# Optimization experiments

Measured on AMD Instinct MI355X. Metric: run time of the kernel, lower is better.

The kernel has to match this reference:

```python
import jax, jax.numpy as jnp
import numpy as np
import math

B, N, DIM = 8, 4096, 768
H, D = 12, 64
STAGES = 3
LN_EPS = 1e-5

def _ln(x, g, b):
    mu = jnp.mean(x, axis=-1, keepdims=True)
    var = jnp.mean(jnp.square(x - mu), axis=-1, keepdims=True)
    return (x - mu) * jax.lax.rsqrt(var + LN_EPS) * g + b

def _mlp(x, W, b, g, be):
    return jax.nn.gelu(_ln(x @ W + b, g, be), approximate=False)

def setup_inputs() -> dict:
    key = jax.random.key(0)
    ks = jax.random.split(key, 16)
    s = lambda i, shape, sc: jax.random.normal(ks[i], shape, jnp.float32) * sc
    return {
        "x": s(0, (B, N, DIM), 1.0),
        "Wq": s(1, (DIM, H * D), DIM ** -0.5),
        "Wk": s(2, (DIM, H * D), DIM ** -0.5),
        "Wv": s(3, (DIM, H * D), DIM ** -0.5),
        "pool_W": s(4, (STAGES, D, D), D ** -0.5),
        "pool_b": jnp.zeros((STAGES, D), jnp.float32),
        "pool_g": jnp.ones((STAGES, D), jnp.float32),
        "pool_be": jnp.zeros((STAGES, D), jnp.float32),
        "exp_W": s(5, (STAGES, D, D), D ** -0.5),
        "exp_b": jnp.zeros((STAGES, D), jnp.float32),
        "exp_g": jnp.ones((STAGES, D), jnp.float32),
        "exp_be": jnp.zeros((STAGES, D), jnp.float32),
        "Wo": s(6, (H * D, DIM), (H * D) ** -0.5),
        "bo": jnp.zeros((DIM,), jnp.float32),
    }

def reference(x, Wq, Wk, Wv, pool_W, pool_b, pool_g, pool_be,
              exp_W, exp_b, exp_g, exp_be, Wo, bo):
    b, n, _ = x.shape
    # project and split heads -> (b, h, n, d)
    def heads(y):
        return y.reshape(b, n, H, D).transpose(0, 2, 1, 3)
    q = heads(x @ Wq)
    k = heads(x @ Wk)
    v = heads(x @ Wv)
    fmap = lambda t: jax.nn.elu(t) + 1.0
    q = fmap(q)
    k = fmap(k)

    kc, vc = k, v
    for i in range(STAGES):
        s = kc.shape[2]
        if s > 1:
            pad = (-s) % 2
            if pad:
                kc = jnp.pad(kc, ((0, 0), (0, 0), (0, pad), (0, 0)))
                vc = jnp.pad(vc, ((0, 0), (0, 0), (0, pad), (0, 0)))
            kc = kc.reshape(b, H, -1, 2, D).mean(axis=3)
            kc = _mlp(kc, pool_W[i], pool_b[i], pool_g[i], pool_be[i])
            vc = vc.reshape(b, H, -1, 2, D).mean(axis=3)

    kc = kc / math.sqrt(kc.shape[2])
    kv = jnp.einsum('bhnd,bhne->bhde', kc, vc)       # (b,h,d,d)
    out = jnp.einsum('bhnd,bhde->bhne', q, kv)       # (b,h,n,d)
    k_sum = kc.sum(axis=2, keepdims=True)            # (b,h,1,d)
    q_k_sum = jnp.sum(q * k_sum, axis=-1, keepdims=True)  # (b,h,n,1)
    out = out / (q_k_sum + 1e-6)

    for i in reversed(range(STAGES)):
        out = _mlp(out, exp_W[i], exp_b[i], exp_g[i], exp_be[i])

    out = out.transpose(0, 2, 1, 3).reshape(b, n, H * D)
    return out @ Wo + bo
```

## Files before the change

kernel.cpp:

```cpp
#include <hip/hip_runtime.h>
#include <math.h>

#define B_   8
#define N_   4096
#define DIM_ 768
#define H_   12
#define D_   64

typedef unsigned short ushort_t;
typedef unsigned int uint_t;
typedef __attribute__((ext_vector_type(8))) short short8;
typedef __attribute__((ext_vector_type(4))) float f32x4;

__device__ __forceinline__ float gelu_exact(float z) {
  return 0.5f * z * (1.f + erff(z * 0.70710678118654752440f));
}

__device__ __forceinline__ ushort_t f2bf(float f) {
  union { float f; unsigned u; } x; x.f = f;
  unsigned r = x.u + 0x7FFFu + ((x.u >> 16) & 1u);
  return (ushort_t)(r >> 16);
}

__device__ __forceinline__ float bf2f(ushort_t h) {
  union { unsigned u; float f; } x; x.u = ((unsigned)h) << 16;
  return x.f;
}

__device__ __forceinline__ void gl_lds16(const ushort_t* g, ushort_t* l) {
  __builtin_amdgcn_global_load_lds(
      (const __attribute__((address_space(1))) void*)g,
      (__attribute__((address_space(3))) void*)l, 16, 0, 0);
}

__global__ __launch_bounds__(256) void transpose_w_bf16(
    const float* __restrict__ src, ushort_t* __restrict__ dst)
{
  __shared__ float t[32][33];
  const int lx = threadIdx.x & 31, ly = threadIdx.x >> 5;
  const int bx = blockIdx.x * 32;
  const int by = blockIdx.y * 32;
  #pragma unroll
  for (int j = 0; j < 32; j += 8)
    t[ly + j][lx] = src[(size_t)(by + ly + j) * 768 + bx + lx];
  __syncthreads();
  #pragma unroll
  for (int j = 0; j < 32; j += 8)
    dst[(size_t)(bx + ly + j) * 768 + by + lx] = f2bf(t[lx][ly + j]);
}

__global__ __launch_bounds__(256) void transpose64_bf16(
    const float* __restrict__ pW, const float* __restrict__ eW,
    ushort_t* __restrict__ dst)
{
  const int m = blockIdx.x;
  const float* src = (m < 3) ? (pW + m * 4096) : (eW + (m - 3) * 4096);
  ushort_t* o = dst + m * 4096;
  for (int i = threadIdx.x; i < 4096; i += 256) {
    const int r = i >> 6, c = i & 63;
    o[c * 64 + r] = f2bf(src[r * 64 + c]);
  }
}

__global__ __launch_bounds__(256) void conv_f32_bf16(
    const float* __restrict__ src, ushort_t* __restrict__ dst)
{
  const int i = blockIdx.x * 256 + threadIdx.x;
  float4 f = ((const float4*)src)[i];
  ushort4 o;
  o.x = f2bf(f.x); o.y = f2bf(f.y); o.z = f2bf(f.z); o.w = f2bf(f.w);
  ((ushort4*)dst)[i] = o;
}

#define GEMM_MAINLOOP(A, Bt, K)                                               \
  __shared__ ushort_t As[128 * 32];                                           \
  __shared__ ushort_t Bs[128 * 32];                                           \
  const int tid = threadIdx.x;                                                \
  const int row0 = blockIdx.y * 128;                                          \
  const int col0 = blockIdx.x * 128;                                          \
  const int sr = tid >> 2;                                                    \
  const int sk = (tid & 3) * 8;                                               \
  const ushort_t* Ag0 = (A) + (size_t)(row0 + sr) * (K) + sk;                 \
  const ushort_t* Ag1 = Ag0 + (size_t)64 * (K);                               \
  const ushort_t* Bg0 = (Bt) + (size_t)(col0 + sr) * (K) + sk;                \
  const ushort_t* Bg1 = Bg0 + (size_t)64 * (K);                               \
  ushort_t* Asw = As + (tid >> 6) * 512;                                      \
  ushort_t* Bsw = Bs + (tid >> 6) * 512;                                      \
  const int w = tid >> 6, lane = tid & 63;                                    \
  const int wm = w >> 1, wn = w & 1;                                          \
  const int qd = lane >> 4, l15 = lane & 15;                                  \
  const int aoff = (wm * 64 + l15) * 32 + qd * 8;                             \
  const int boff = (wn * 64 + l15) * 32 + qd * 8;                             \
  f32x4 acc[4][4] = {};                                                       \
  for (int k0 = 0; k0 < (K); k0 += 32) {                                      \
    __syncthreads();                                                          \
    gl_lds16(Ag0 + k0, Asw);                                                  \
    gl_lds16(Ag1 + k0, Asw + 2048);                                           \
    gl_lds16(Bg0 + k0, Bsw);                                                  \
    gl_lds16(Bg1 + k0, Bsw + 2048);                                           \
    __syncthreads();                                                          \
    short8 af[4], bfr[4];                                                     \
    _Pragma("unroll")                                                         \
    for (int mt = 0; mt < 4; ++mt) af[mt] = *(const short8*)&As[aoff + mt * 512]; \
    _Pragma("unroll")                                                         \
    for (int nt = 0; nt < 4; ++nt) bfr[nt] = *(const short8*)&Bs[boff + nt * 512]; \
    _Pragma("unroll")                                                         \
    for (int mt = 0; mt < 4; ++mt)                                            \
      _Pragma("unroll")                                                       \
      for (int nt = 0; nt < 4; ++nt)                                          \
        acc[mt][nt] = __builtin_amdgcn_mfma_f32_16x16x32_bf16(                \
            af[mt], bfr[nt], acc[mt][nt], 0, 0, 0);                           \
  }

__global__ __launch_bounds__(256) void gemm_qkv(
    const ushort_t* __restrict__ A, const ushort_t* __restrict__ Bt,
    ushort_t* __restrict__ qo, ushort_t* __restrict__ ko, float* __restrict__ vco)
{
  GEMM_MAINLOOP(A, Bt, 768)
  const int sel = col0 / 768;
  const int colbase = (col0 % 768) + wn * 64;
  if (sel < 2) {
    ushort_t* o = (sel == 0) ? qo : ko;
    #pragma unroll
    for (int mt = 0; mt < 4; ++mt) {
      #pragma unroll
      for (int nt = 0; nt < 4; ++nt) {
        const int cg = colbase + nt * 16 + l15;
        #pragma unroll
        for (int r = 0; r < 4; ++r) {
          const int rg = row0 + wm * 64 + mt * 16 + qd * 4 + r;
          const float vv = acc[mt][nt][r];
          const float e = (vv > 0.f) ? vv + 1.f : expf(vv);
          o[(size_t)rg * 768 + cg] = f2bf(e);
        }
      }
    }
  } else {
    const int b = row0 >> 12;
    const int hh = colbase >> 6;
    const int n8base = ((row0 & 4095) >> 3) + wm * 8 + (qd >> 1);
    #pragma unroll
    for (int mt = 0; mt < 4; ++mt) {
      #pragma unroll
      for (int nt = 0; nt < 4; ++nt) {
        float s = acc[mt][nt][0] + acc[mt][nt][1] + acc[mt][nt][2] + acc[mt][nt][3];
        s += __shfl_xor(s, 16, 64);
        if (!(qd & 1)) {
          const int n8 = n8base + mt * 2;
          const int d = nt * 16 + l15;
          vco[(((size_t)b * 12 + hh) * 512 + n8) * 64 + d] = 0.125f * s;
        }
      }
    }
  }
}

__global__ __launch_bounds__(256) void gemm_out(
    const ushort_t* __restrict__ A, const ushort_t* __restrict__ Bt,
    const float* __restrict__ bo, float* __restrict__ C)
{
  GEMM_MAINLOOP(A, Bt, 768)
  #pragma unroll
  for (int mt = 0; mt < 4; ++mt) {
    #pragma unroll
    for (int nt = 0; nt < 4; ++nt) {
      const int cg = col0 + wn * 64 + nt * 16 + l15;
      #pragma unroll
      for (int r = 0; r < 4; ++r) {
        const int rg = row0 + wm * 64 + mt * 16 + qd * 4 + r;
        C[(size_t)rg * 768 + cg] = acc[mt][nt][r] + bo[cg];
      }
    }
  }
}

__global__ __launch_bounds__(256) void pool_mfma(
    const ushort_t* __restrict__ in, ushort_t* __restrict__ out,
    int n_out, long h_stride, int ts, long in_bs, long out_bs,
    const ushort_t* __restrict__ Wt, const float* __restrict__ bias,
    const float* __restrict__ g, const float* __restrict__ be)
{
  __shared__ ushort_t Wl[64 * 72];
  __shared__ ushort_t tl[128 * 72];
  const int tid = threadIdx.x;
  const int h = blockIdx.y;
  const int bb = blockIdx.z;
  const int row0 = blockIdx.x * 128;
  in  += (size_t)bb * in_bs;
  out += (size_t)bb * out_bs;

  {
    const uint_t* ws = (const uint_t*)Wt;
    for (int i = tid; i < 2048; i += 256) {
      const int r = i >> 5, c = i & 31;
      ((uint_t*)(Wl + r * 72))[c] = ws[i];
    }
  }
  #pragma unroll
  for (int j = 0; j < 4; ++j) {
    const int idx = j * 256 + tid;
    const int rl = idx >> 3, ch = idx & 7;
    const ushort_t* p = in + (size_t)h * h_stride + (size_t)(2 * (row0 + rl)) * ts + ch * 8;
    short8 a = *(const short8*)p;
    short8 b2 = *(const short8*)(p + ts);
    short8 o;
    #pragma unroll
    for (int e = 0; e < 8; ++e)
      o[e] = (short)f2bf(0.5f * (bf2f((ushort_t)a[e]) + bf2f((ushort_t)b2[e])));
    *(short8*)&tl[rl * 72 + ch * 8] = o;
  }
  __syncthreads();

  const int w = tid >> 6, lane = tid & 63;
  const int quad = lane >> 4, l15 = lane & 15;

  float bv[4], gv[4], bev[4];
  #pragma unroll
  for (int nt = 0; nt < 4; ++nt) {
    const int c = nt * 16 + l15;
    bv[nt] = bias[c]; gv[nt] = g[c]; bev[nt] = be[c];
  }
  f32x4 a2[2][4];
  #pragma unroll
  for (int mt = 0; mt < 2; ++mt)
    #pragma unroll
    for (int nt = 0; nt < 4; ++nt)
      a2[mt][nt] = f32x4{bv[nt], bv[nt], bv[nt], bv[nt]};

  #pragma unroll
  for (int ks = 0; ks < 2; ++ks) {
    short8 af[2], bfr[4];
    #pragma unroll
    for (int mt = 0; mt < 2; ++mt)
      af[mt] = *(const short8*)&tl[(w * 32 + mt * 16 + l15) * 72 + ks * 32 + quad * 8];
    #pragma unroll
    for (int nt = 0; nt < 4; ++nt)
      bfr[nt] = *(const short8*)&Wl[(nt * 16 + l15) * 72 + ks * 32 + quad * 8];
    #pragma unroll
    for (int mt = 0; mt < 2; ++mt)
      #pragma unroll
      for (int nt = 0; nt < 4; ++nt)
        a2[mt][nt] = __builtin_amdgcn_mfma_f32_16x16x32_bf16(af[mt], bfr[nt], a2[mt][nt], 0, 0, 0);
  }

  #pragma unroll
  for (int mt = 0; mt < 2; ++mt)
    #pragma unroll
    for (int r = 0; r < 4; ++r) {
      float sum = a2[mt][0][r] + a2[mt][1][r] + a2[mt][2][r] + a2[mt][3][r];
      #pragma unroll
      for (int m = 1; m < 16; m <<= 1) sum += __shfl_xor(sum, m, 64);
      const float mu = sum * 0.015625f;
      float dv[4], var = 0.f;
      #pragma unroll
      for (int nt = 0; nt < 4; ++nt) { dv[nt] = a2[mt][nt][r] - mu; var += dv[nt] * dv[nt]; }
      #pragma unroll
      for (int m = 1; m < 16; m <<= 1) var += __shfl_xor(var, m, 64);
      const float rstd = rsqrtf(var * 0.015625f + 1e-5f);
      const int rg = row0 + w * 32 + mt * 16 + quad * 4 + r;
      #pragma unroll
      for (int nt = 0; nt < 4; ++nt) {
        const float z = dv[nt] * rstd * gv[nt] + bev[nt];
        out[((size_t)h * n_out + rg) * 64 + nt * 16 + l15] = f2bf(gelu_exact(z));
      }
    }
}

__global__ __launch_bounds__(256) void kv_part_kernel(
    const ushort_t* __restrict__ kc, const float* __restrict__ vc,
    float* __restrict__ kvp, float* __restrict__ ksp)
{
  __shared__ float ks[32 * 64];
  __shared__ float vs[32 * 64];
  const int tid = threadIdx.x;
  const int h = blockIdx.x;
  const int c = blockIdx.y;
  const int bb = blockIdx.z;
  kc  += (size_t)bb * 393216;
  vc  += (size_t)bb * 393216;
  kvp += (size_t)bb * 786432;
  ksp += (size_t)bb * 12288;
  const ushort_t* kp = kc + ((size_t)h * 512 + c * 32) * 64;
  const float* vp = vc + ((size_t)h * 512 + c * 32) * 64;
  #pragma unroll
  for (int i = 0; i < 2; ++i) {
    ushort4 u = ((const ushort4*)kp)[tid + 256 * i];
    float4 f; f.x = bf2f(u.x); f.y = bf2f(u.y); f.z = bf2f(u.z); f.w = bf2f(u.w);
    ((float4*)ks)[tid + 256 * i] = f;
    ((float4*)vs)[tid + 256 * i] = ((const float4*)vp)[tid + 256 * i];
  }
  __syncthreads();

  const int e = tid & 63;
  const int dg = tid >> 6;
  float acc[16] = {};
  float accs = 0.f;
  for (int nn = 0; nn < 32; ++nn) {
    const float vv = vs[nn * 64 + e];
    #pragma unroll
    for (int j = 0; j < 16; ++j)
      acc[j] += ks[nn * 64 + dg * 16 + j] * vv;
    if (tid < 64) accs += ks[nn * 64 + tid];
  }
  float* o = kvp + ((size_t)h * 16 + c) * 4096;
  #pragma unroll
  for (int j = 0; j < 16; ++j)
    o[(dg * 16 + j) * 64 + e] = acc[j];
  if (tid < 64) ksp[(h * 16 + c) * 64 + tid] = accs;
}

__global__ __launch_bounds__(256) void kv_reduce_t(
    const float* __restrict__ kvp, const float* __restrict__ ksp,
    ushort_t* __restrict__ kvxT)
{
  const int bb = blockIdx.y;
  kvp  += (size_t)bb * 786432;
  ksp  += (size_t)bb * 12288;
  kvxT += (size_t)bb * 61440;
  const int idx = blockIdx.x * 256 + threadIdx.x;
  const int h = idx / 5120;
  const int rem = idx - h * 5120;
  const int er = rem >> 6, d = rem & 63;
  const float scale = 0.044194173824159216f;
  float val = 0.f;
  if (er < 64) {
    float s = 0.f;
    #pragma unroll
    for (int c = 0; c < 16; ++c) s += kvp[((size_t)h * 16 + c) * 4096 + d * 64 + er];
    val = s * scale;
  } else if (er == 64) {
    float s = 0.f;
    #pragma unroll
    for (int c = 0; c < 16; ++c) s += ksp[(h * 16 + c) * 64 + d];
    val = s * scale;
  }
  kvxT[idx] = f2bf(val);
}

__global__ __launch_bounds__(256) void attn_exp_mfma(
    const ushort_t* __restrict__ q16, const ushort_t* __restrict__ kvxT,
    const ushort_t* __restrict__ eWt,
    const float* __restrict__ eb, const float* __restrict__ eg,
    const float* __restrict__ ebe, ushort_t* __restrict__ out16)
{
  __shared__ ushort_t kvl[80 * 72];
  __shared__ ushort_t Wl[3 * 64 * 72];
  __shared__ ushort_t tl[128 * 72];
  const int tid = threadIdx.x;
  const int h = blockIdx.y;
  const int bb = blockIdx.z;
  const int row0 = blockIdx.x * 128;
  q16   += (size_t)bb * 3145728;
  out16 += (size_t)bb * 3145728;
  kvxT  += (size_t)bb * 61440;

  {
    const uint_t* src = (const uint_t*)(kvxT + (size_t)h * 5120);
    for (int i = tid; i < 2560; i += 256) {
      const int r = i >> 5, c = i & 31;
      ((uint_t*)(kvl + r * 72))[c] = src[i];
    }
    const uint_t* ws = (const uint_t*)eWt;
    for (int i = tid; i < 6144; i += 256) {
      const int s = i >> 11, rem = i & 2047, r = rem >> 5, c = rem & 31;
      ((uint_t*)(Wl + (s * 64 + r) * 72))[c] = ws[i];
    }
  }
  __syncthreads();

  const int w = tid >> 6, lane = tid & 63;
  const int quad = lane >> 4, l15 = lane & 15;

  f32x4 acc[2][5] = {};
  #pragma unroll
  for (int ks = 0; ks < 2; ++ks) {
    short8 af[2], bfr[5];
    #pragma unroll
    for (int mt = 0; mt < 2; ++mt) {
      const int rg = row0 + w * 32 + mt * 16 + l15;
      af[mt] = *(const short8*)(q16 + (size_t)rg * 768 + h * 64 + ks * 32 + quad * 8);
    }
    #pragma unroll
    for (int nt = 0; nt < 5; ++nt)
      bfr[nt] = *(const short8*)&kvl[(nt * 16 + l15) * 72 + ks * 32 + quad * 8];
    #pragma unroll
    for (int mt = 0; mt < 2; ++mt)
      #pragma unroll
      for (int nt = 0; nt < 5; ++nt)
        acc[mt][nt] = __builtin_amdgcn_mfma_f32_16x16x32_bf16(af[mt], bfr[nt], acc[mt][nt], 0, 0, 0);
  }

  float t[2][4][4];
  #pragma unroll
  for (int mt = 0; mt < 2; ++mt)
    #pragma unroll
    for (int r = 0; r < 4; ++r) {
      const float den = __shfl(acc[mt][4][r], lane & 48, 64) + 1e-6f;
      const float inv = 1.f / den;
      #pragma unroll
      for (int nt = 0; nt < 4; ++nt)
        t[mt][nt][r] = acc[mt][nt][r] * inv;
    }

  for (int s = 2; s >= 0; --s) {
    __syncthreads();
    #pragma unroll
    for (int mt = 0; mt < 2; ++mt)
      #pragma unroll
      for (int nt = 0; nt < 4; ++nt)
        #pragma unroll
        for (int r = 0; r < 4; ++r)
          tl[(w * 32 + mt * 16 + quad * 4 + r) * 72 + nt * 16 + l15] = f2bf(t[mt][nt][r]);
    __syncthreads();

    float bv[4], gv[4], bev[4];
    #pragma unroll
    for (int nt = 0; nt < 4; ++nt) {
      const int c = s * 64 + nt * 16 + l15;
      bv[nt] = eb[c]; gv[nt] = eg[c]; bev[nt] = ebe[c];
    }
    f32x4 a2[2][4];
    #pragma unroll
    for (int mt = 0; mt < 2; ++mt)
      #pragma unroll
      for (int nt = 0; nt < 4; ++nt)
        a2[mt][nt] = f32x4{bv[nt], bv[nt], bv[nt], bv[nt]};

    #pragma unroll
    for (int ks = 0; ks < 2; ++ks) {
      short8 af[2], bfr[4];
      #pragma unroll
      for (int mt = 0; mt < 2; ++mt)
        af[mt] = *(const short8*)&tl[(w * 32 + mt * 16 + l15) * 72 + ks * 32 + quad * 8];
      #pragma unroll
      for (int nt = 0; nt < 4; ++nt)
        bfr[nt] = *(const short8*)&Wl[(s * 64 + nt * 16 + l15) * 72 + ks * 32 + quad * 8];
      #pragma unroll
      for (int mt = 0; mt < 2; ++mt)
        #pragma unroll
        for (int nt = 0; nt < 4; ++nt)
          a2[mt][nt] = __builtin_amdgcn_mfma_f32_16x16x32_bf16(af[mt], bfr[nt], a2[mt][nt], 0, 0, 0);
    }

    #pragma unroll
    for (int mt = 0; mt < 2; ++mt)
      #pragma unroll
      for (int r = 0; r < 4; ++r) {
        float sum = a2[mt][0][r] + a2[mt][1][r] + a2[mt][2][r] + a2[mt][3][r];
        #pragma unroll
        for (int m = 1; m < 16; m <<= 1) sum += __shfl_xor(sum, m, 64);
        const float mu = sum * 0.015625f;
        float dv[4], var = 0.f;
        #pragma unroll
        for (int nt = 0; nt < 4; ++nt) { dv[nt] = a2[mt][nt][r] - mu; var += dv[nt] * dv[nt]; }
        #pragma unroll
        for (int m = 1; m < 16; m <<= 1) var += __shfl_xor(var, m, 64);
        const float rstd = rsqrtf(var * 0.015625f + 1e-5f);
        #pragma unroll
        for (int nt = 0; nt < 4; ++nt) {
          const float z = dv[nt] * rstd * gv[nt] + bev[nt];
          t[mt][nt][r] = gelu_exact(z);
        }
      }
  }

  #pragma unroll
  for (int mt = 0; mt < 2; ++mt)
    #pragma unroll
    for (int nt = 0; nt < 4; ++nt)
      #pragma unroll
      for (int r = 0; r < 4; ++r) {
        const int rg = row0 + w * 32 + mt * 16 + quad * 4 + r;
        out16[(size_t)rg * 768 + h * 64 + nt * 16 + l15] = f2bf(t[mt][nt][r]);
      }
}

extern "C" void kernel_launch(void* const* d_in, const int* in_sizes, int n_in,
                              void* d_out, int out_size, void* d_ws, size_t ws_size,
                              hipStream_t stream)
{
  const float* x   = (const float*)d_in[0];
  const float* Wq  = (const float*)d_in[1];
  const float* Wk  = (const float*)d_in[2];
  const float* Wv  = (const float*)d_in[3];
  const float* pW  = (const float*)d_in[4];
  const float* pb  = (const float*)d_in[5];
  const float* pg  = (const float*)d_in[6];
  const float* pbe = (const float*)d_in[7];
  const float* eW  = (const float*)d_in[8];
  const float* eb  = (const float*)d_in[9];
  const float* eg  = (const float*)d_in[10];
  const float* ebe = (const float*)d_in[11];
  const float* Wo  = (const float*)d_in[12];
  const float* bo  = (const float*)d_in[13];
  float* outp = (float*)d_out;

  unsigned char* wsb = (unsigned char*)d_ws;
  ushort_t* WqkvT = (ushort_t*)(wsb + 0);
  ushort_t* WoT   = (ushort_t*)(wsb + 3538944);
  ushort_t* Wt6   = (ushort_t*)(wsb + 4718592);
  const size_t CB   = 4767744;
  const size_t PERB = 26075136;

  int NB;
  if      (ws_size >= CB + 8 * PERB) NB = 8;
  else if (ws_size >= CB + 4 * PERB) NB = 4;
  else if (ws_size >= CB + 2 * PERB) NB = 2;
  else if (ws_size >= CB + 1 * PERB) NB = 1;
  else return;

  unsigned char* cb = wsb + CB;
  ushort_t* xb16 = (ushort_t*)(cb);
  ushort_t* q16  = (ushort_t*)(cb + (size_t)NB *  6291456);
  ushort_t* k16  = (ushort_t*)(cb + (size_t)NB * 12582912);
  float*    vc   = (float*)   (cb + (size_t)NB * 18874368);
  ushort_t* kc_a = (ushort_t*)(cb + (size_t)NB * 20447232);
  ushort_t* kc_b = (ushort_t*)(cb + (size_t)NB * 23592960);
  ushort_t* kc_c = (ushort_t*)(cb + (size_t)NB * 25165824);
  ushort_t* kvxT = (ushort_t*)(cb + (size_t)NB * 25952256);
  float* kvp = (float*)k16;
  float* ksp = (float*)((unsigned char*)k16 + (size_t)NB * 3145728);
  ushort_t* ao16 = xb16;

  const ushort_t* pWt = Wt6;
  const ushort_t* eWt = Wt6 + 3 * 4096;
  const size_t SB = (size_t)N_ * DIM_;

  transpose_w_bf16<<<dim3(24, 24), 256, 0, stream>>>(Wq, WqkvT);
  transpose_w_bf16<<<dim3(24, 24), 256, 0, stream>>>(Wk, WqkvT + 768 * 768);
  transpose_w_bf16<<<dim3(24, 24), 256, 0, stream>>>(Wv, WqkvT + 2 * 768 * 768);
  transpose_w_bf16<<<dim3(24, 24), 256, 0, stream>>>(Wo, WoT);
  transpose64_bf16<<<6, 256, 0, stream>>>(pW, eW, Wt6);

  for (int b0 = 0; b0 < B_; b0 += NB) {
    const float* xc = x + (size_t)b0 * SB;
    float* oc = outp + (size_t)b0 * SB;

    conv_f32_bf16<<<NB * 3072, 256, 0, stream>>>(xc, xb16);
    gemm_qkv<<<dim3(18, NB * 32), 256, 0, stream>>>(xb16, WqkvT, q16, k16, vc);

    pool_mfma<<<dim3(16, 12, NB), 256, 0, stream>>>(k16, kc_a, 2048, 64L, 768,
        3145728L, 1572864L, pWt, pb, pg, pbe);
    pool_mfma<<<dim3(8, 12, NB), 256, 0, stream>>>(kc_a, kc_b, 1024, 131072L, 64,
        1572864L, 786432L, pWt + 4096, pb + 64, pg + 64, pbe + 64);
    pool_mfma<<<dim3(4, 12, NB), 256, 0, stream>>>(kc_b, kc_c, 512, 65536L, 64,
        786432L, 393216L, pWt + 8192, pb + 128, pg + 128, pbe + 128);

    kv_part_kernel<<<dim3(12, 16, NB), 256, 0, stream>>>(kc_c, vc, kvp, ksp);
    kv_reduce_t<<<dim3(240, NB), 256, 0, stream>>>(kvp, ksp, kvxT);

    attn_exp_mfma<<<dim3(32, 12, NB), 256, 0, stream>>>(q16, kvxT, eWt,
                                                        eb, eg, ebe, ao16);

    gemm_out<<<dim3(6, NB * 32), 256, 0, stream>>>(ao16, WoT, bo, oc);
  }
}
```

Baseline: 705.4 us.

## Double-buffer GEMM LDS tiles and remap workgroup IDs across XCDs

The shared GEMM main loop now uses two LDS buffers per operand. The global-to-LDS load for the next 32-wide K slice is issued before the MFMA compute on the current slice, so load latency can overlap compute. The workgroup index is also permuted in groups of 8 so that neighbouring tiles land on the same XCD, aiming for better L2 reuse. This doubles LDS use per block, which may lower occupancy, and the remap assumes the grid size is divisible by 8.

```diff
diff --git a/kernel.cpp b/kernel.cpp
--- a/kernel.cpp
+++ b/kernel.cpp
@@ -72,44 +72,57 @@
   ((ushort4*)dst)[i] = o;
 }
 
+#define GEMM_STAGE(kk, As_, Bs_)                                              \
+    gl_lds16(Ag0 + (kk), (As_) + stoff_);                                     \
+    gl_lds16(Ag1 + (kk), (As_) + stoff_ + 2048);                              \
+    gl_lds16(Bg0 + (kk), (Bs_) + stoff_);                                     \
+    gl_lds16(Bg1 + (kk), (Bs_) + stoff_ + 2048);
+
+#define GEMM_COMPUTE(As_, Bs_)                                                \
+  { short8 af[4], bfr[4];                                                     \
+    _Pragma("unroll")                                                         \
+    for (int mt = 0; mt < 4; ++mt) af[mt] = *(const short8*)&(As_)[aoff + mt * 512]; \
+    _Pragma("unroll")                                                         \
+    for (int nt = 0; nt < 4; ++nt) bfr[nt] = *(const short8*)&(Bs_)[boff + nt * 512]; \
+    _Pragma("unroll")                                                         \
+    for (int mt = 0; mt < 4; ++mt)                                            \
+      _Pragma("unroll")                                                       \
+      for (int nt = 0; nt < 4; ++nt)                                          \
+        acc[mt][nt] = __builtin_amdgcn_mfma_f32_16x16x32_bf16(                \
+            af[mt], bfr[nt], acc[mt][nt], 0, 0, 0); }
+
 #define GEMM_MAINLOOP(A, Bt, K)                                               \
-  __shared__ ushort_t As[128 * 32];                                           \
-  __shared__ ushort_t Bs[128 * 32];                                           \
+  __shared__ ushort_t As0[128 * 32];                                          \
+  __shared__ ushort_t As1[128 * 32];                                          \
+  __shared__ ushort_t Bs0[128 * 32];                                          \
+  __shared__ ushort_t Bs1[128 * 32];                                          \
   const int tid = threadIdx.x;                                                \
-  const int row0 = blockIdx.y * 128;                                          \
-  const int col0 = blockIdx.x * 128;                                          \
+  const int nwg_ = (int)(gridDim.x * gridDim.y);                              \
+  const int wgid0_ = (int)(blockIdx.y * gridDim.x + blockIdx.x);              \
+  const int wgid_ = (wgid0_ & 7) * (nwg_ >> 3) + (wgid0_ >> 3);               \
+  const int row0 = (wgid_ / (int)gridDim.x) * 128;                            \
+  const int col0 = (wgid_ % (int)gridDim.x) * 128;                            \
   const int sr = tid >> 2;                                                    \
   const int sk = (tid & 3) * 8;                                               \
   const ushort_t* Ag0 = (A) + (size_t)(row0 + sr) * (K) + sk;                 \
   const ushort_t* Ag1 = Ag0 + (size_t)64 * (K);                               \
   const ushort_t* Bg0 = (Bt) + (size_t)(col0 + sr) * (K) + sk;                \
   const ushort_t* Bg1 = Bg0 + (size_t)64 * (K);                               \
-  ushort_t* Asw = As + (tid >> 6) * 512;                                      \
-  ushort_t* Bsw = Bs + (tid >> 6) * 512;                                      \
+  const int stoff_ = (tid >> 6) * 512;                                        \
   const int w = tid >> 6, lane = tid & 63;                                    \
   const int wm = w >> 1, wn = w & 1;                                          \
   const int qd = lane >> 4, l15 = lane & 15;                                  \
   const int aoff = (wm * 64 + l15) * 32 + qd * 8;                             \
   const int boff = (wn * 64 + l15) * 32 + qd * 8;                             \
   f32x4 acc[4][4] = {};                                                       \
-  for (int k0 = 0; k0 < (K); k0 += 32) {                                      \
+  GEMM_STAGE(0, As0, Bs0)                                                     \
+  for (int k0 = 0; k0 < (K); k0 += 64) {                                      \
     __syncthreads();                                                          \
-    gl_lds16(Ag0 + k0, Asw);                                                  \
-    gl_lds16(Ag1 + k0, Asw + 2048);                                           \
-    gl_lds16(Bg0 + k0, Bsw);                                                  \
-    gl_lds16(Bg1 + k0, Bsw + 2048);                                           \
+    GEMM_STAGE(k0 + 32, As1, Bs1)                                             \
+    GEMM_COMPUTE(As0, Bs0)                                                    \
     __syncthreads();                                                          \
-    short8 af[4], bfr[4];                                                     \
-    _Pragma("unroll")                                                         \
-    for (int mt = 0; mt < 4; ++mt) af[mt] = *(const short8*)&As[aoff + mt * 512]; \
-    _Pragma("unroll")                                                         \
-    for (int nt = 0; nt < 4; ++nt) bfr[nt] = *(const short8*)&Bs[boff + nt * 512]; \
-    _Pragma("unroll")                                                         \
-    for (int mt = 0; mt < 4; ++mt)                                            \
-      _Pragma("unroll")                                                       \
-      for (int nt = 0; nt < 4; ++nt)                                          \
-        acc[mt][nt] = __builtin_amdgcn_mfma_f32_16x16x32_bf16(                \
-            af[mt], bfr[nt], acc[mt][nt], 0, 0, 0);                           \
+    if (k0 + 64 < (K)) { GEMM_STAGE(k0 + 64, As0, Bs0) }                      \
+    GEMM_COMPUTE(As1, Bs1)                                                    \
   }
 
 __global__ __launch_bounds__(256) void gemm_qkv(
```

New measurement: 698.0 us. Within noise of the previous version (-1.0%).

## Pool x before V projection and remap GEMM workgroups across XCDs

Applied to the files above, without the earlier changes.

Since V is only used after three stages of mean-pooling by 2, x is now averaged over groups of 8 rows first. The V projection then runs on an 8x smaller input in a separate small GEMM, which removes 1/3 of the QKV GEMM's FLOPs. The GEMM macro also remaps workgroup IDs so consecutive tiles interleave across the 8 XCDs, and the ELU path uses the fast __expf. Averaging bf16 x before the bf16 conversion changes rounding slightly, and the new kernel adds an extra pass over x.

```diff
diff --git a/kernel.cpp b/kernel.cpp
--- a/kernel.cpp
+++ b/kernel.cpp
@@ -72,12 +72,34 @@
   ((ushort4*)dst)[i] = o;
 }
 
+__global__ __launch_bounds__(256) void pool8_x(
+    const ushort_t* __restrict__ xb, ushort_t* __restrict__ x8)
+{
+  const int idx = blockIdx.x * 256 + threadIdx.x;
+  const int r = idx / 96, gc = idx - r * 96;
+  const ushort_t* p = xb + (size_t)(8 * r) * 768 + gc * 8;
+  float s[8] = {};
+  #pragma unroll
+  for (int j = 0; j < 8; ++j) {
+    short8 v = *(const short8*)(p + (size_t)j * 768);
+    #pragma unroll
+    for (int e = 0; e < 8; ++e) s[e] += bf2f((ushort_t)v[e]);
+  }
+  short8 o;
+  #pragma unroll
+  for (int e = 0; e < 8; ++e) o[e] = (short)f2bf(0.125f * s[e]);
+  *(short8*)(x8 + (size_t)r * 768 + gc * 8) = o;
+}
+
 #define GEMM_MAINLOOP(A, Bt, K)                                               \
   __shared__ ushort_t As[128 * 32];                                           \
   __shared__ ushort_t Bs[128 * 32];                                           \
   const int tid = threadIdx.x;                                                \
-  const int row0 = blockIdx.y * 128;                                          \
-  const int col0 = blockIdx.x * 128;                                          \
+  const int nwg_ = (int)(gridDim.x * gridDim.y);                              \
+  const int wgid0_ = (int)(blockIdx.y * gridDim.x + blockIdx.x);              \
+  const int wgid_ = (wgid0_ & 7) * (nwg_ >> 3) + (wgid0_ >> 3);               \
+  const int row0 = (wgid_ / (int)gridDim.x) * 128;                            \
+  const int col0 = (wgid_ % (int)gridDim.x) * 128;                            \
   const int sr = tid >> 2;                                                    \
   const int sk = (tid & 3) * 8;                                               \
   const ushort_t* Ag0 = (A) + (size_t)(row0 + sr) * (K) + sk;                 \
@@ -114,42 +136,44 @@
 
 __global__ __launch_bounds__(256) void gemm_qkv(
     const ushort_t* __restrict__ A, const ushort_t* __restrict__ Bt,
-    ushort_t* __restrict__ qo, ushort_t* __restrict__ ko, float* __restrict__ vco)
+    ushort_t* __restrict__ qo, ushort_t* __restrict__ ko)
 {
   GEMM_MAINLOOP(A, Bt, 768)
   const int sel = col0 / 768;
   const int colbase = (col0 % 768) + wn * 64;
-  if (sel < 2) {
-    ushort_t* o = (sel == 0) ? qo : ko;
-    #pragma unroll
-    for (int mt = 0; mt < 4; ++mt) {
-      #pragma unroll
-      for (int nt = 0; nt < 4; ++nt) {
-        const int cg = colbase + nt * 16 + l15;
-        #pragma unroll
-        for (int r = 0; r < 4; ++r) {
-          const int rg = row0 + wm * 64 + mt * 16 + qd * 4 + r;
-          const float vv = acc[mt][nt][r];
-          const float e = (vv > 0.f) ? vv + 1.f : expf(vv);
-          o[(size_t)rg * 768 + cg] = f2bf(e);
-        }
+  ushort_t* o = (sel == 0) ? qo : ko;
+  #pragma unroll
+  for (int mt = 0; mt < 4; ++mt) {
+    #pragma unroll
+    for (int nt = 0; nt < 4; ++nt) {
+      const int cg = colbase + nt * 16 + l15;
+      #pragma unroll
+      for (int r = 0; r < 4; ++r) {
+        const int rg = row0 + wm * 64 + mt * 16 + qd * 4 + r;
+        const float vv = acc[mt][nt][r];
+        const float e = (vv > 0.f) ? vv + 1.f : __expf(vv);
+        o[(size_t)rg * 768 + cg] = f2bf(e);
       }
     }
-  } else {
-    const int b = row0 >> 12;
-    const int hh = colbase >> 6;
-    const int n8base = ((row0 & 4095) >> 3) + wm * 8 + (qd >> 1);
-    #pragma unroll
-    for (int mt = 0; mt < 4; ++mt) {
-      #pragma unroll
-      for (int nt = 0; nt < 4; ++nt) {
-        float s = acc[mt][nt][0] + acc[mt][nt][1] + acc[mt][nt][2] + acc[mt][nt][3];
-        s += __shfl_xor(s, 16, 64);
-        if (!(qd & 1)) {
-          const int n8 = n8base + mt * 2;
-          const int d = nt * 16 + l15;
-          vco[(((size_t)b * 12 + hh) * 512 + n8) * 64 + d] = 0.125f * s;
-        }
+  }
+}
+
+__global__ __launch_bounds__(256) void gemm_v(
+    const ushort_t* __restrict__ A, const ushort_t* __restrict__ Bt,
+    float* __restrict__ vco)
+{
+  GEMM_MAINLOOP(A, Bt, 768)
+  #pragma unroll
+  for (int mt = 0; mt < 4; ++mt) {
+    #pragma unroll
+    for (int nt = 0; nt < 4; ++nt) {
+      const int cg = col0 + wn * 64 + nt * 16 + l15;
+      const int hh = cg >> 6, d = cg & 63;
+      #pragma unroll
+      for (int r = 0; r < 4; ++r) {
+        const int rg = row0 + wm * 64 + mt * 16 + qd * 4 + r;
+        const int b = rg >> 9, n = rg & 511;
+        vco[(((size_t)b * 12 + hh) * 512 + n) * 64 + d] = acc[mt][nt][r];
       }
     }
   }
@@ -500,7 +524,7 @@
   ushort_t* WoT   = (ushort_t*)(wsb + 3538944);
   ushort_t* Wt6   = (ushort_t*)(wsb + 4718592);
   const size_t CB   = 4767744;
-  const size_t PERB = 26075136;
+  const size_t PERB = 26861568;
 
   int NB;
   if      (ws_size >= CB + 8 * PERB) NB = 8;
@@ -518,6 +542,7 @@
   ushort_t* kc_b = (ushort_t*)(cb + (size_t)NB * 23592960);
   ushort_t* kc_c = (ushort_t*)(cb + (size_t)NB * 25165824);
   ushort_t* kvxT = (ushort_t*)(cb + (size_t)NB * 25952256);
+  ushort_t* x8   = (ushort_t*)(cb + (size_t)NB * 26075136);
   float* kvp = (float*)k16;
   float* ksp = (float*)((unsigned char*)k16 + (size_t)NB * 3145728);
   ushort_t* ao16 = xb16;
@@ -532,12 +557,16 @@
   transpose_w_bf16<<<dim3(24, 24), 256, 0, stream>>>(Wo, WoT);
   transpose64_bf16<<<6, 256, 0, stream>>>(pW, eW, Wt6);
 
+  const ushort_t* WvT = WqkvT + 2 * 768 * 768;
+
   for (int b0 = 0; b0 < B_; b0 += NB) {
     const float* xc = x + (size_t)b0 * SB;
     float* oc = outp + (size_t)b0 * SB;
 
     conv_f32_bf16<<<NB * 3072, 256, 0, stream>>>(xc, xb16);
-    gemm_qkv<<<dim3(18, NB * 32), 256, 0, stream>>>(xb16, WqkvT, q16, k16, vc);
+    pool8_x<<<NB * 192, 256, 0, stream>>>(xb16, x8);
+    gemm_qkv<<<dim3(12, NB * 32), 256, 0, stream>>>(xb16, WqkvT, q16, k16);
+    gemm_v<<<dim3(6, NB * 4), 256, 0, stream>>>(x8, WvT, vc);
 
     pool_mfma<<<dim3(16, 12, NB), 256, 0, stream>>>(k16, kc_a, 2048, 64L, 768,
         3145728L, 1572864L, pWt, pb, pg, pbe);
```

After: 678.1 us. 1.04x faster.
